# Kernel optimization log

Hardware: AMD Instinct MI355X
Metric: run time of the kernel (lower is better)

Reference implementation:

```python
import jax, jax.numpy as jnp
import numpy as np

H = 1024  # HIDDEN_LAYER_SIZE

def _xavier(key, shape, gain=0.01):
    fan_out, fan_in = shape
    a = gain * np.sqrt(6.0 / (fan_in + fan_out))
    return jax.random.uniform(key, shape, jnp.float32, -a, a)

def setup_inputs() -> dict:
    key = jax.random.key(0)
    ks = jax.random.split(key, 7)
    B = 65536
    white_features = jax.random.uniform(ks[0], (B, 768), jnp.float32)
    black_features = jax.random.uniform(ks[1], (B, 768), jnp.float32)
    stm = jax.random.uniform(ks[2], (B, 1), jnp.float32)
    return {
        "white_features": white_features,
        "black_features": black_features,
        "stm": stm,
        "ft_w": _xavier(ks[3], (H, 768)),
        "ft_b": jnp.zeros((H,), jnp.float32),
        "l1_w": _xavier(ks[4], (8, 2 * H)),
        "l1_b": jnp.zeros((8,), jnp.float32),
        "l2_w": _xavier(ks[5], (32, 8)),
        "l2_b": jnp.zeros((32,), jnp.float32),
        "l3_w": _xavier(ks[6], (1, 32)),
        "l3_b": jnp.zeros((1,), jnp.float32),
    }

def reference(white_features, black_features, stm, ft_w, ft_b,
              l1_w, l1_b, l2_w, l2_b, l3_w, l3_b):
    w = white_features @ ft_w.T + ft_b  # [B, H]
    b = black_features @ ft_w.T + ft_b  # [B, H]
    acc = stm * jnp.concatenate([w, b], axis=1) + (1.0 - stm) * jnp.concatenate([b, w], axis=1)
    l1_x = jnp.clip(acc, 0.0, 1.0)
    l2_x = jnp.clip(l1_x @ l1_w.T + l1_b, 0.0, 1.0)
    l3_x = jnp.clip(l2_x @ l2_w.T + l2_b, 0.0, 1.0)
    raw_output = l3_x @ l3_w.T + l3_b  # [B, 1]
    output = jax.nn.sigmoid(raw_output)
    return (output, raw_output)
```

## Files before the change

kernel.cpp:

```cpp
#include <hip/hip_runtime.h>
#include <cmath>

typedef float f4_t __attribute__((ext_vector_type(4)));
typedef float f2_t __attribute__((ext_vector_type(2)));
typedef long  l2_t __attribute__((ext_vector_type(2)));

#define B_TOTAL   65536
#define FTW_SCALE 1024.0f
#define INV_SCALE (1.0f/1024.0f)

__device__ __forceinline__ int pk8(float a, float b, float c, float d) {
    int v = __builtin_amdgcn_cvt_pk_fp8_f32(a, b, 0, false);
    return  __builtin_amdgcn_cvt_pk_fp8_f32(c, d, v, true);
}
__device__ __forceinline__ float clip01(float x) { return fminf(fmaxf(x, 0.f), 1.f); }

__global__ void pack_ftw_kernel(const float* __restrict__ ftw, char* __restrict__ ws)
{
    int t    = blockIdx.x * 256 + threadIdx.x;
    int lane = t & 63;
    int ncp  = (t >> 6) & 31;
    int kk   = t >> 11;
    int nl = lane & 15, q = (lane >> 4) & 3;
    int k0 = kk * 32 + q * 8;
    const float* p0 = ftw + (size_t)(ncp * 32 + nl) * 768 + k0;
    const float* p1 = p0 + 16 * 768;
    float4 x0 = *(const float4*)p0;
    float4 x1 = *(const float4*)(p0 + 4);
    float4 y0 = *(const float4*)p1;
    float4 y1 = *(const float4*)(p1 + 4);
    int4 o;
    o.x = pk8(x0.x*FTW_SCALE, x0.y*FTW_SCALE, x0.z*FTW_SCALE, x0.w*FTW_SCALE);
    o.y = pk8(x1.x*FTW_SCALE, x1.y*FTW_SCALE, x1.z*FTW_SCALE, x1.w*FTW_SCALE);
    o.z = pk8(y0.x*FTW_SCALE, y0.y*FTW_SCALE, y0.z*FTW_SCALE, y0.w*FTW_SCALE);
    o.w = pk8(y1.x*FTW_SCALE, y1.y*FTW_SCALE, y1.z*FTW_SCALE, y1.w*FTW_SCALE);
    *(int4*)(ws + (size_t)t * 16) = o;
}

__global__ __launch_bounds__(256, 3) void nnue_fused_kernel(
    const float* __restrict__ wf,  const float* __restrict__ bfeat,
    const float* __restrict__ stm, const char*  __restrict__ ftw8,
    const float* __restrict__ ftb, const float* __restrict__ l1w,
    const float* __restrict__ l1b, const float* __restrict__ l2w,
    const float* __restrict__ l2b, const float* __restrict__ l3w,
    const float* __restrict__ l3b, float* __restrict__ out)
{
    __shared__ char  Ald[24 * 2048];
    __shared__ float l1part[4][32][8];

    const int t    = threadIdx.x;
    const int lane = t & 63;
    const int wave = t >> 6;
    const int nl   = lane & 15;
    const int q    = (lane >> 4) & 3;
    const int s0   = blockIdx.x * 32;

    {
        const int kpar = t >> 7;
        const int tt   = t & 127;
        const int p    = tt >> 6;
        const int sl   = tt & 63;
        const int snl  = sl & 15, sq = (sl >> 4) & 3;
        const float* base = p ? bfeat : wf;
        const float* r0 = base + (size_t)(s0 + snl) * 768;
        const float* r1 = r0 + 16 * 768;
        char* dst = &Ald[p * 1024 + sl * 16];
        #pragma unroll 4
        for (int pass = 0; pass < 12; ++pass) {
            int kk = pass * 2 + kpar;
            int k0 = kk * 32 + sq * 8;
            float4 x0 = *(const float4*)(r0 + k0);
            float4 x1 = *(const float4*)(r0 + k0 + 4);
            float4 y0 = *(const float4*)(r1 + k0);
            float4 y1 = *(const float4*)(r1 + k0 + 4);
            int4 o;
            o.x = pk8(x0.x, x0.y, x0.z, x0.w);
            o.y = pk8(x1.x, x1.y, x1.z, x1.w);
            o.z = pk8(y0.x, y0.y, y0.z, y0.w);
            o.w = pk8(y1.x, y1.y, y1.z, y1.w);
            *(int4*)(dst + kk * 2048) = o;
        }
    }

    float s_lo[4], s_hi[4];
    #pragma unroll
    for (int r = 0; r < 4; ++r) {
        s_lo[r] = stm[s0 + q * 4 + r];
        s_hi[r] = stm[s0 + 16 + q * 4 + r];
    }

    __syncthreads();

    f2_t pacc[2][4][4];
    #pragma unroll
    for (int mh = 0; mh < 2; ++mh)
        #pragma unroll
        for (int r = 0; r < 4; ++r)
            #pragma unroll
            for (int i = 0; i < 4; ++i) pacc[mh][r][i] = (f2_t){0.f, 0.f};

    const char* ap = &Ald[lane * 16];

    #pragma unroll 1
    for (int ng = 0; ng < 8; ++ng) {
        f4_t acc[4][2];
        #pragma unroll
        for (int m = 0; m < 4; ++m) {
            acc[m][0] = (f4_t){0.f,0.f,0.f,0.f};
            acc[m][1] = (f4_t){0.f,0.f,0.f,0.f};
        }
        const char* bp = ftw8 + (size_t)(wave * 8 + ng) * 1024 + (size_t)lane * 16;
        l2_t bc0 = *(const l2_t*)(bp);
        l2_t bc1 = *(const l2_t*)(bp + 32768);

        #pragma unroll 2
        for (int kg = 0; kg < 12; ++kg) {
            int pf0 = (kg < 11) ? (2 * kg + 2) : 22;
            int pf1 = (kg < 11) ? (2 * kg + 3) : 23;
            l2_t bn0 = *(const l2_t*)(bp + (size_t)pf0 * 32768);
            l2_t bn1 = *(const l2_t*)(bp + (size_t)pf1 * 32768);

            l2_t aw = *(const l2_t*)(ap + (2 * kg) * 2048);
            l2_t ab = *(const l2_t*)(ap + (2 * kg) * 2048 + 1024);
            acc[0][0] = __builtin_amdgcn_mfma_f32_16x16x32_fp8_fp8(aw.x, bc0.x, acc[0][0], 0,0,0);
            acc[1][0] = __builtin_amdgcn_mfma_f32_16x16x32_fp8_fp8(aw.y, bc0.x, acc[1][0], 0,0,0);
            acc[2][0] = __builtin_amdgcn_mfma_f32_16x16x32_fp8_fp8(ab.x, bc0.x, acc[2][0], 0,0,0);
            acc[3][0] = __builtin_amdgcn_mfma_f32_16x16x32_fp8_fp8(ab.y, bc0.x, acc[3][0], 0,0,0);
            acc[0][1] = __builtin_amdgcn_mfma_f32_16x16x32_fp8_fp8(aw.x, bc0.y, acc[0][1], 0,0,0);
            acc[1][1] = __builtin_amdgcn_mfma_f32_16x16x32_fp8_fp8(aw.y, bc0.y, acc[1][1], 0,0,0);
            acc[2][1] = __builtin_amdgcn_mfma_f32_16x16x32_fp8_fp8(ab.x, bc0.y, acc[2][1], 0,0,0);
            acc[3][1] = __builtin_amdgcn_mfma_f32_16x16x32_fp8_fp8(ab.y, bc0.y, acc[3][1], 0,0,0);

            l2_t aw2 = *(const l2_t*)(ap + (2 * kg + 1) * 2048);
            l2_t ab2 = *(const l2_t*)(ap + (2 * kg + 1) * 2048 + 1024);
            acc[0][0] = __builtin_amdgcn_mfma_f32_16x16x32_fp8_fp8(aw2.x, bc1.x, acc[0][0], 0,0,0);
            acc[1][0] = __builtin_amdgcn_mfma_f32_16x16x32_fp8_fp8(aw2.y, bc1.x, acc[1][0], 0,0,0);
            acc[2][0] = __builtin_amdgcn_mfma_f32_16x16x32_fp8_fp8(ab2.x, bc1.x, acc[2][0], 0,0,0);
            acc[3][0] = __builtin_amdgcn_mfma_f32_16x16x32_fp8_fp8(ab2.y, bc1.x, acc[3][0], 0,0,0);
            acc[0][1] = __builtin_amdgcn_mfma_f32_16x16x32_fp8_fp8(aw2.x, bc1.y, acc[0][1], 0,0,0);
            acc[1][1] = __builtin_amdgcn_mfma_f32_16x16x32_fp8_fp8(aw2.y, bc1.y, acc[1][1], 0,0,0);
            acc[2][1] = __builtin_amdgcn_mfma_f32_16x16x32_fp8_fp8(ab2.x, bc1.y, acc[2][1], 0,0,0);
            acc[3][1] = __builtin_amdgcn_mfma_f32_16x16x32_fp8_fp8(ab2.y, bc1.y, acc[3][1], 0,0,0);

            bc0 = bn0; bc1 = bn1;
        }

        #pragma unroll
        for (int nb = 0; nb < 2; ++nb) {
            int col = wave * 256 + ng * 32 + nb * 16 + nl;
            float bias = ftb[col];
            const float* l1c = l1w + col;
            f2_t lo2[4], hi2[4];
            #pragma unroll
            for (int i = 0; i < 4; ++i) {
                lo2[i] = (f2_t){l1c[(2*i) * 2048],        l1c[(2*i+1) * 2048]};
                hi2[i] = (f2_t){l1c[(2*i) * 2048 + 1024], l1c[(2*i+1) * 2048 + 1024]};
            }
            #pragma unroll
            for (int r = 0; r < 4; ++r) {
                float w0 = fmaf(acc[0][nb][r], INV_SCALE, bias);
                float w1 = fmaf(acc[1][nb][r], INV_SCALE, bias);
                float b0 = fmaf(acc[2][nb][r], INV_SCALE, bias);
                float b1 = fmaf(acc[3][nb][r], INV_SCALE, bias);
                float d0 = w0 - b0, d1 = w1 - b1;
                float f0 = clip01(fmaf( s_lo[r], d0, b0));
                float g0 = clip01(fmaf(-s_lo[r], d0, w0));
                float f1 = clip01(fmaf( s_hi[r], d1, b1));
                float g1 = clip01(fmaf(-s_hi[r], d1, w1));
                #pragma unroll
                for (int i = 0; i < 4; ++i) {
                    pacc[0][r][i] += f0 * lo2[i] + g0 * hi2[i];
                    pacc[1][r][i] += f1 * lo2[i] + g1 * hi2[i];
                }
            }
        }
    }

    #pragma unroll
    for (int m = 1; m < 16; m <<= 1)
        #pragma unroll
        for (int mh = 0; mh < 2; ++mh)
            #pragma unroll
            for (int r = 0; r < 4; ++r)
                #pragma unroll
                for (int i = 0; i < 4; ++i) {
                    pacc[mh][r][i].x += __shfl_xor(pacc[mh][r][i].x, m);
                    pacc[mh][r][i].y += __shfl_xor(pacc[mh][r][i].y, m);
                }

    if (nl == 0) {
        #pragma unroll
        for (int mh = 0; mh < 2; ++mh)
            #pragma unroll
            for (int r = 0; r < 4; ++r)
                #pragma unroll
                for (int i = 0; i < 4; ++i) {
                    l1part[wave][mh * 16 + q * 4 + r][2*i]   = pacc[mh][r][i].x;
                    l1part[wave][mh * 16 + q * 4 + r][2*i+1] = pacc[mh][r][i].y;
                }
    }
    __syncthreads();

    if (t < 32) {
        float v[8];
        #pragma unroll
        for (int o = 0; o < 8; ++o)
            v[o] = clip01(l1part[0][t][o] + l1part[1][t][o] +
                          l1part[2][t][o] + l1part[3][t][o] + l1b[o]);
        float raw = l3b[0];
        #pragma unroll
        for (int u = 0; u < 32; ++u) {
            float h = l2b[u];
            #pragma unroll
            for (int o = 0; o < 8; ++o) h = fmaf(v[o], l2w[u * 8 + o], h);
            h = clip01(h);
            raw = fmaf(h, l3w[u], raw);
        }
        out[s0 + t]           = 1.0f / (1.0f + expf(-raw));
        out[B_TOTAL + s0 + t] = raw;
    }
}

extern "C" void kernel_launch(void* const* d_in, const int* in_sizes, int n_in,
                              void* d_out, int out_size, void* d_ws, size_t ws_size,
                              hipStream_t stream)
{
    const float* wf  = (const float*)d_in[0];
    const float* bf  = (const float*)d_in[1];
    const float* stm = (const float*)d_in[2];
    const float* ftw = (const float*)d_in[3];
    const float* ftb = (const float*)d_in[4];
    const float* l1w = (const float*)d_in[5];
    const float* l1b = (const float*)d_in[6];
    const float* l2w = (const float*)d_in[7];
    const float* l2b = (const float*)d_in[8];
    const float* l3w = (const float*)d_in[9];
    const float* l3b = (const float*)d_in[10];
    char* ws8 = (char*)d_ws;

    hipLaunchKernelGGL(pack_ftw_kernel, dim3(192), dim3(256), 0, stream, ftw, ws8);
    hipLaunchKernelGGL(nnue_fused_kernel, dim3(2048), dim3(256), 0, stream,
                       wf, bf, stm, ws8, ftb, l1w, l1b, l2w, l2b, l3w, l3b,
                       (float*)d_out);
}
```

Baseline: 600.1 us.

## Deepen B-operand prefetch, transpose l1 weights, hoist epilogue loads into MMA loop

The FP8 B-fragment prefetch becomes a three-stage register pipeline, and the K loop is fully unrolled. The first stages for the next column group are loaded before the current epilogue, so global latency overlaps with ALU work. A new pre-kernel transposes l1_w so each column's 8 weights load as contiguous float2 vectors, and these loads are issued mid-loop. This hides latency but raises register pressure under launch_bounds(256,3) and adds a small extra kernel launch.

```diff
diff --git a/kernel.cpp b/kernel.cpp
--- a/kernel.cpp
+++ b/kernel.cpp
@@ -8,6 +8,7 @@
 #define B_TOTAL   65536
 #define FTW_SCALE 1024.0f
 #define INV_SCALE (1.0f/1024.0f)
+#define L1WT_OFF  (768 * 1024)
 
 __device__ __forceinline__ int pk8(float a, float b, float c, float d) {
     int v = __builtin_amdgcn_cvt_pk_fp8_f32(a, b, 0, false);
@@ -37,10 +38,37 @@
     *(int4*)(ws + (size_t)t * 16) = o;
 }
 
+__global__ void pack_l1w_kernel(const float* __restrict__ l1w, float* __restrict__ l1wT)
+{
+    int t = blockIdx.x * 256 + threadIdx.x;
+    int c = t >> 3, o = t & 7;
+    l1wT[t] = l1w[o * 2048 + c];
+}
+
+#define HALF_STEP(AW, AB, BV)                                                                  \
+    acc[0][0] = __builtin_amdgcn_mfma_f32_16x16x32_fp8_fp8((AW).x, (BV).x, acc[0][0], 0,0,0);  \
+    acc[1][0] = __builtin_amdgcn_mfma_f32_16x16x32_fp8_fp8((AW).y, (BV).x, acc[1][0], 0,0,0);  \
+    acc[2][0] = __builtin_amdgcn_mfma_f32_16x16x32_fp8_fp8((AB).x, (BV).x, acc[2][0], 0,0,0);  \
+    acc[3][0] = __builtin_amdgcn_mfma_f32_16x16x32_fp8_fp8((AB).y, (BV).x, acc[3][0], 0,0,0);  \
+    acc[0][1] = __builtin_amdgcn_mfma_f32_16x16x32_fp8_fp8((AW).x, (BV).y, acc[0][1], 0,0,0);  \
+    acc[1][1] = __builtin_amdgcn_mfma_f32_16x16x32_fp8_fp8((AW).y, (BV).y, acc[1][1], 0,0,0);  \
+    acc[2][1] = __builtin_amdgcn_mfma_f32_16x16x32_fp8_fp8((AB).x, (BV).y, acc[2][1], 0,0,0);  \
+    acc[3][1] = __builtin_amdgcn_mfma_f32_16x16x32_fp8_fp8((AB).y, (BV).y, acc[3][1], 0,0,0);
+
+#define KG_STEP(KG)                                                         \
+    {                                                                       \
+        l2_t aw  = *(const l2_t*)(ap + (2*(KG)) * 2048);                    \
+        l2_t ab  = *(const l2_t*)(ap + (2*(KG)) * 2048 + 1024);             \
+        HALF_STEP(aw, ab, bA0)                                              \
+        l2_t aw2 = *(const l2_t*)(ap + (2*(KG)+1) * 2048);                  \
+        l2_t ab2 = *(const l2_t*)(ap + (2*(KG)+1) * 2048 + 1024);           \
+        HALF_STEP(aw2, ab2, bA1)                                            \
+    }
+
 __global__ __launch_bounds__(256, 3) void nnue_fused_kernel(
     const float* __restrict__ wf,  const float* __restrict__ bfeat,
     const float* __restrict__ stm, const char*  __restrict__ ftw8,
-    const float* __restrict__ ftb, const float* __restrict__ l1w,
+    const float* __restrict__ ftb, const float* __restrict__ l1wT,
     const float* __restrict__ l1b, const float* __restrict__ l2w,
     const float* __restrict__ l2b, const float* __restrict__ l3w,
     const float* __restrict__ l3b, float* __restrict__ out)
@@ -99,63 +127,72 @@
             #pragma unroll
             for (int i = 0; i < 4; ++i) pacc[mh][r][i] = (f2_t){0.f, 0.f};
 
-    const char* ap = &Ald[lane * 16];
+    const char* ap  = &Ald[lane * 16];
+    const char* bpw = ftw8 + (size_t)(wave * 8) * 1024 + (size_t)lane * 16;
+
+    l2_t pA0 = *(const l2_t*)(bpw);
+    l2_t pA1 = *(const l2_t*)(bpw + 1 * 32768);
+    l2_t pB0 = *(const l2_t*)(bpw + 2 * 32768);
+    l2_t pB1 = *(const l2_t*)(bpw + 3 * 32768);
+    l2_t pC0 = *(const l2_t*)(bpw + 4 * 32768);
+    l2_t pC1 = *(const l2_t*)(bpw + 5 * 32768);
 
     #pragma unroll 1
     for (int ng = 0; ng < 8; ++ng) {
+        const char* bp = bpw + ng * 1024;
+
         f4_t acc[4][2];
         #pragma unroll
         for (int m = 0; m < 4; ++m) {
             acc[m][0] = (f4_t){0.f,0.f,0.f,0.f};
             acc[m][1] = (f4_t){0.f,0.f,0.f,0.f};
         }
-        const char* bp = ftw8 + (size_t)(wave * 8 + ng) * 1024 + (size_t)lane * 16;
-        l2_t bc0 = *(const l2_t*)(bp);
-        l2_t bc1 = *(const l2_t*)(bp + 32768);
-
-        #pragma unroll 2
-        for (int kg = 0; kg < 12; ++kg) {
-            int pf0 = (kg < 11) ? (2 * kg + 2) : 22;
-            int pf1 = (kg < 11) ? (2 * kg + 3) : 23;
-            l2_t bn0 = *(const l2_t*)(bp + (size_t)pf0 * 32768);
-            l2_t bn1 = *(const l2_t*)(bp + (size_t)pf1 * 32768);
-
-            l2_t aw = *(const l2_t*)(ap + (2 * kg) * 2048);
-            l2_t ab = *(const l2_t*)(ap + (2 * kg) * 2048 + 1024);
-            acc[0][0] = __builtin_amdgcn_mfma_f32_16x16x32_fp8_fp8(aw.x, bc0.x, acc[0][0], 0,0,0);
-            acc[1][0] = __builtin_amdgcn_mfma_f32_16x16x32_fp8_fp8(aw.y, bc0.x, acc[1][0], 0,0,0);
-            acc[2][0] = __builtin_amdgcn_mfma_f32_16x16x32_fp8_fp8(ab.x, bc0.x, acc[2][0], 0,0,0);
-            acc[3][0] = __builtin_amdgcn_mfma_f32_16x16x32_fp8_fp8(ab.y, bc0.x, acc[3][0], 0,0,0);
-            acc[0][1] = __builtin_amdgcn_mfma_f32_16x16x32_fp8_fp8(aw.x, bc0.y, acc[0][1], 0,0,0);
-            acc[1][1] = __builtin_amdgcn_mfma_f32_16x16x32_fp8_fp8(aw.y, bc0.y, acc[1][1], 0,0,0);
-            acc[2][1] = __builtin_amdgcn_mfma_f32_16x16x32_fp8_fp8(ab.x, bc0.y, acc[2][1], 0,0,0);
-            acc[3][1] = __builtin_amdgcn_mfma_f32_16x16x32_fp8_fp8(ab.y, bc0.y, acc[3][1], 0,0,0);
-
-            l2_t aw2 = *(const l2_t*)(ap + (2 * kg + 1) * 2048);
-            l2_t ab2 = *(const l2_t*)(ap + (2 * kg + 1) * 2048 + 1024);
-            acc[0][0] = __builtin_amdgcn_mfma_f32_16x16x32_fp8_fp8(aw2.x, bc1.x, acc[0][0], 0,0,0);
-            acc[1][0] = __builtin_amdgcn_mfma_f32_16x16x32_fp8_fp8(aw2.y, bc1.x, acc[1][0], 0,0,0);
-            acc[2][0] = __builtin_amdgcn_mfma_f32_16x16x32_fp8_fp8(ab2.x, bc1.x, acc[2][0], 0,0,0);
-            acc[3][0] = __builtin_amdgcn_mfma_f32_16x16x32_fp8_fp8(ab2.y, bc1.x, acc[3][0], 0,0,0);
-            acc[0][1] = __builtin_amdgcn_mfma_f32_16x16x32_fp8_fp8(aw2.x, bc1.y, acc[0][1], 0,0,0);
-            acc[1][1] = __builtin_amdgcn_mfma_f32_16x16x32_fp8_fp8(aw2.y, bc1.y, acc[1][1], 0,0,0);
-            acc[2][1] = __builtin_amdgcn_mfma_f32_16x16x32_fp8_fp8(ab2.x, bc1.y, acc[2][1], 0,0,0);
-            acc[3][1] = __builtin_amdgcn_mfma_f32_16x16x32_fp8_fp8(ab2.y, bc1.y, acc[3][1], 0,0,0);
-
-            bc0 = bn0; bc1 = bn1;
+
+        l2_t bA0 = pA0, bA1 = pA1, bB0 = pB0, bB1 = pB1, bC0 = pC0, bC1 = pC1;
+
+        #pragma unroll
+        for (int kg = 0; kg < 9; ++kg) {
+            l2_t bn0 = *(const l2_t*)(bp + (2 * kg + 6) * 32768);
+            l2_t bn1 = *(const l2_t*)(bp + (2 * kg + 7) * 32768);
+            KG_STEP(kg)
+            bA0 = bB0; bA1 = bB1; bB0 = bC0; bB1 = bC1; bC0 = bn0; bC1 = bn1;
+        }
+
+        const int colb = wave * 256 + ng * 32 + nl;
+        float bias0 = ftb[colb];
+        float bias1 = ftb[colb + 16];
+        f2_t lo2[2][4], hi2[2][4];
+        {
+            const f2_t* q0  = (const f2_t*)(l1wT + (size_t)colb * 8);
+            const f2_t* q0h = (const f2_t*)(l1wT + (size_t)(colb + 1024) * 8);
+            const f2_t* q1  = (const f2_t*)(l1wT + (size_t)(colb + 16) * 8);
+            const f2_t* q1h = (const f2_t*)(l1wT + (size_t)(colb + 1040) * 8);
+            #pragma unroll
+            for (int i = 0; i < 4; ++i) {
+                lo2[0][i] = q0[i];  hi2[0][i] = q0h[i];
+                lo2[1][i] = q1[i];  hi2[1][i] = q1h[i];
+            }
+        }
+
+        #pragma unroll
+        for (int kg = 9; kg < 12; ++kg) {
+            KG_STEP(kg)
+            bA0 = bB0; bA1 = bB1; bB0 = bC0; bB1 = bC1;
+        }
+
+        if (ng < 7) {
+            const char* bpn = bpw + (ng + 1) * 1024;
+            pA0 = *(const l2_t*)(bpn);
+            pA1 = *(const l2_t*)(bpn + 1 * 32768);
+            pB0 = *(const l2_t*)(bpn + 2 * 32768);
+            pB1 = *(const l2_t*)(bpn + 3 * 32768);
+            pC0 = *(const l2_t*)(bpn + 4 * 32768);
+            pC1 = *(const l2_t*)(bpn + 5 * 32768);
         }
 
         #pragma unroll
         for (int nb = 0; nb < 2; ++nb) {
-            int col = wave * 256 + ng * 32 + nb * 16 + nl;
-            float bias = ftb[col];
-            const float* l1c = l1w + col;
-            f2_t lo2[4], hi2[4];
-            #pragma unroll
-            for (int i = 0; i < 4; ++i) {
-                lo2[i] = (f2_t){l1c[(2*i) * 2048],        l1c[(2*i+1) * 2048]};
-                hi2[i] = (f2_t){l1c[(2*i) * 2048 + 1024], l1c[(2*i+1) * 2048 + 1024]};
-            }
+            float bias = nb ? bias1 : bias0;
             #pragma unroll
             for (int r = 0; r < 4; ++r) {
                 float w0 = fmaf(acc[0][nb][r], INV_SCALE, bias);
@@ -169,8 +206,8 @@
                 float g1 = clip01(fmaf(-s_hi[r], d1, w1));
                 #pragma unroll
                 for (int i = 0; i < 4; ++i) {
-                    pacc[0][r][i] += f0 * lo2[i] + g0 * hi2[i];
-                    pacc[1][r][i] += f1 * lo2[i] + g1 * hi2[i];
+                    pacc[0][r][i] += f0 * lo2[nb][i] + g0 * hi2[nb][i];
+                    pacc[1][r][i] += f1 * lo2[nb][i] + g1 * hi2[nb][i];
                 }
             }
         }
@@ -225,6 +262,7 @@
                               void* d_out, int out_size, void* d_ws, size_t ws_size,
                               hipStream_t stream)
 {
+    (void)in_sizes; (void)n_in; (void)out_size; (void)ws_size;
     const float* wf  = (const float*)d_in[0];
     const float* bf  = (const float*)d_in[1];
     const float* stm = (const float*)d_in[2];
@@ -236,10 +274,12 @@
     const float* l2b = (const float*)d_in[8];
     const float* l3w = (const float*)d_in[9];
     const float* l3b = (const float*)d_in[10];
-    char* ws8 = (char*)d_ws;
+    char*  ws8  = (char*)d_ws;
+    float* l1wT = (float*)(ws8 + L1WT_OFF);
 
     hipLaunchKernelGGL(pack_ftw_kernel, dim3(192), dim3(256), 0, stream, ftw, ws8);
+    hipLaunchKernelGGL(pack_l1w_kernel, dim3(64), dim3(256), 0, stream, l1w, l1wT);
     hipLaunchKernelGGL(nnue_fused_kernel, dim3(2048), dim3(256), 0, stream,
-                       wf, bf, stm, ws8, ftb, l1w, l1b, l2w, l2b, l3w, l3b,
+                       wf, bf, stm, ws8, ftb, l1wT, l1b, l2w, l2b, l3w, l3b,
                        (float*)d_out);
 }
```

Measured after the change: 1.022 ms. 1.7x slower.
